# Kernel optimization log

Measured on AMD Instinct MI355X. Metric: run time of the kernel, lower is better.

## Reference

```python
import jax, jax.numpy as jnp
import numpy as np

# ---- static config (mirrors __init__) ----
OMEGAS = [5.0, 7.0, 9.0, 12.0, 16.0, 22.0, 30.0, 40.0]
XI = 0.05
DT = 0.01
UJ_U1 = 0.01

_decay = (1.0 / (2.0 * np.pi * XI)) * np.log(1.0 / UJ_U1)  # cycles to decay to uj_u1
VALID_W = [int(2.0 * np.pi / w / np.sqrt(1.0 - XI ** 2) * _decay / DT) for w in OMEGAS]
KER = [2 * a - 1 for a in VALID_W]  # per-channel duhamel kernel size (odd)
MAXK = max(KER)
OUT_CH = len(OMEGAS)


def _build_irfs(log_omegas):
    """Analytic impulse-response filter bank, shape [OUT_CH, 1, MAXK]."""
    omegas = jnp.clip(jnp.exp(log_omegas), 0.01, 1000.0)
    sq = jnp.sqrt(jnp.float32(1.0 - XI ** 2))
    rows = []
    for i in range(OUT_CH):  # small fixed loop over channels (distinct static lengths)
        W, K = VALID_W[i], KER[i]
        tt = jnp.arange(W, dtype=jnp.float32) * DT
        omegaD = omegas[i] * sq
        irf = (1.0 / omegaD) * jnp.exp(-XI * omegas[i] * tt) * jnp.sin(omegaD * tt)
        w = jnp.concatenate([irf[::-1], jnp.zeros((K // 2,), jnp.float32)])  # len K
        addpad = MAXK - K  # even, since K and MAXK are both odd
        w = jnp.pad(w, (addpad // 2, addpad // 2))
        rows.append(w)
    return jnp.stack(rows)[:, None, :]  # [O, 1, MAXK]


def setup_inputs() -> dict:
    key = jax.random.key(0)
    x = jax.random.normal(key, (16, 1, 65536), dtype=jnp.float32)
    log_omegas = jnp.log(jnp.asarray(OMEGAS, dtype=jnp.float32))
    return {"inputs": x, "log_omegas": log_omegas}


def reference(inputs, log_omegas):
    irfs = _build_irfs(log_omegas)  # [O,1,MAXK]
    pad = MAXK // 2
    xp = jnp.pad(inputs, ((0, 0), (0, 0), (pad, pad)))
    # torch conv1d is cross-correlation == lax conv (no kernel flip)
    return jax.lax.conv_general_dilated(
        xp, irfs, window_strides=(1,), padding='VALID',
        dimension_numbers=('NCH', 'OIH', 'NCH'))
```

## Files before the change

### kernel.cpp

```cpp
#include <hip/hip_runtime.h>
#include <math.h>


#define N_SAMP  65536
#define NB      16
#define NO      8
#define NT      512
#define LBLK    4096
#define LOOKB   3904
#define TQ      2000

constexpr int CW[NO]  = {1844, 1317, 1024, 768, 576, 419, 307, 230};
constexpr int CHS[NO] = {32, 24, 20, 16, 12, 8, 8, 4};

__device__ __forceinline__ int P(int q) { return q ^ ((q >> 3) & 7); }

__device__ __forceinline__ float rfl(float x) {
    return __int_as_float(__builtin_amdgcn_readfirstlane(__float_as_int(x)));
}

template<int O>
__device__ __forceinline__ void duh_wave(const float* __restrict__ lw,
                                         float* __restrict__ out,
                                         const float* __restrict__ tile,
                                         float* __restrict__ yw,
                                         int b, int n0, int lane)
{
    constexpr int W  = CW[O];
    constexpr int Wu = (W + 3) & ~3;
    constexpr int E  = Wu - W;
    constexpr int QW = Wu / 4;
    constexpr int HS = CHS[O];
    constexpr int HQ = HS / 4;

    const float omf  = fminf(fmaxf(__expf(lw[O]), 0.01f), 1000.0f);
    const float omD  = omf * 0.99874921777190895f;
    const float th   = omD * 0.01f;
    const float alph = 0.0005f * omf;
    const float r1   = __expf(-alph);
    const float gr = rfl(r1 * __cosf(th)), gi = rfl(r1 * __sinf(th));
    const float rW   = __expf(-alph * (float)W);
    const float aW   = th * (float)W;
    const float binv = 1.0f / omD;
    const float c1   = rfl(binv);
    const float c2   = rfl(binv * rW * __cosf(aW));
    const float cei  = rfl(-binv * rW * __sinf(aW));

    float g2r_ = gr*gr - gi*gi,         g2i_ = 2.f*gr*gi;
    float g3r_ = g2r_*gr - g2i_*gi,     g3i_ = g2r_*gi + g2i_*gr;
    float g4r_ = g2r_*g2r_ - g2i_*g2i_, g4i_ = 2.f*g2r_*g2i_;
    const float G2r = rfl(g2r_), G2i = rfl(g2i_);
    const float G3r = rfl(g3r_), G3i = rfl(g3i_);
    const float G4r = rfl(g4r_), G4i = rfl(g4i_);

    float Mor[7], Moi[7];
    {
        const float rl = __expf(-alph * 32.f);
        const float al = th * 32.f;
        float pr = rl * __cosf(al), pq = rl * __sinf(al);
#pragma unroll
        for (int k = 0; k < 7; ++k) {
            Mor[k] = rfl(pr); Moi[k] = rfl(pq);
            const float nr = pr*pr - pq*pq, ni = 2.f*pr*pq;
            pr = nr; pq = ni;
        }
    }
    float Mhr[6], Mhi[6];
    {
        const float rl = __expf(-alph * (float)HS);
        const float al = th * (float)HS;
        float pr = rl * __cosf(al), pq = rl * __sinf(al);
#pragma unroll
        for (int k = 0; k < 6; ++k) {
            Mhr[k] = rfl(pr); Mhi[k] = rfl(pq);
            const float nr = pr*pr - pq*pq, ni = 2.f*pr*pq;
            pr = nr; pq = ni;
        }
    }
    float plr = 1.f, pli = 0.f;
#pragma unroll
    for (int k = 0; k < 6; ++k) {
        if ((lane >> k) & 1) {
            const float nr = plr*Mor[k] - pli*Moi[k];
            const float ni = plr*Moi[k] + pli*Mor[k];
            plr = nr; pli = ni;
        }
    }

#define LDQ(q) (*(const float4*)&tile[4 * P(q)])
#define DSEL(e0,e1,e2,e3,d0,dn)                                              \
    if constexpr (E == 0)      { e0=d0.x; e1=d0.y; e2=d0.z; e3=d0.w; }       \
    else if constexpr (E == 1) { e0=d0.y; e1=d0.z; e2=d0.w; e3=dn.x; }       \
    else if constexpr (E == 2) { e0=d0.z; e1=d0.w; e2=dn.x; e3=dn.y; }       \
    else                       { e0=d0.w; e1=dn.x; e2=dn.y; e3=dn.z; }
#define STEP(xa, xc)                                              \
    {                                                             \
        const float er = fmaf(-c2, (xc), c1 * (xa));              \
        const float ei = cei * (xc);                              \
        const float nr = fmaf(gr, Br, fmaf(-gi, Bi, er));         \
        const float ni = fmaf(gi, Br, fmaf( gr, Bi, ei));         \
        Br = nr; Bi = ni;                                         \
    }

    float Cr, Ci;
    {
        float Br = 0.f, Bi = 0.f;
        const int q1 = 976 - 16 * HS + HQ * lane;
        const int q2 = q1 - QW;
        float4 d0 = LDQ(q2);
#pragma unroll
        for (int m = 0; m < HQ; ++m) {
            const float4 s1 = LDQ(q1 + m);
            const float4 dn = LDQ(q2 + m + 1);
            float e0, e1, e2, e3;
            DSEL(e0, e1, e2, e3, d0, dn);
            STEP(s1.x, e0); STEP(s1.y, e1); STEP(s1.z, e2); STEP(s1.w, e3);
            d0 = dn;
        }
        float Sr = Br, Si = Bi;
#pragma unroll
        for (int k = 0; k < 6; ++k) {
            const int d = 1 << k;
            const float ur = __shfl_up(Sr, d, 64);
            const float ui = __shfl_up(Si, d, 64);
            if (lane >= d) {
                const float nr = fmaf(Mhr[k], ur, fmaf(-Mhi[k], ui, Sr));
                const float ni = fmaf(Mhr[k], ui, fmaf( Mhi[k], ur, Si));
                Sr = nr; Si = ni;
            }
        }
        Cr = rfl(__shfl(Sr, 63, 64));
        Ci = rfl(__shfl(Si, 63, 64));
    }

#pragma unroll
    for (int s = 0; s < 2; ++s) {
        const int q1 = 976 + 512 * s + 8 * lane;
        const int q2 = q1 - QW;

        float4 lz[8];
        float Br = 0.f, Bi = 0.f;
        float4 d0 = LDQ(q2);
#pragma unroll
        for (int m = 0; m < 8; ++m) {
            const float4 s1 = LDQ(q1 + m);
            const float4 dn = LDQ(q2 + m + 1);
            float e0, e1, e2, e3;
            DSEL(e0, e1, e2, e3, d0, dn);
            float4 lq;
            STEP(s1.x, e0); lq.x = Bi;
            STEP(s1.y, e1); lq.y = Bi;
            STEP(s1.z, e2); lq.z = Bi;
            STEP(s1.w, e3); lq.w = Bi;
            lz[m] = lq;
            d0 = dn;
        }

        float Sr = Br, Si = Bi;
#pragma unroll
        for (int k = 0; k < 6; ++k) {
            const int d = 1 << k;
            const float ur = __shfl_up(Sr, d, 64);
            const float ui = __shfl_up(Si, d, 64);
            if (lane >= d) {
                const float nr = fmaf(Mor[k], ur, fmaf(-Moi[k], ui, Sr));
                const float ni = fmaf(Mor[k], ui, fmaf( Moi[k], ur, Si));
                Sr = nr; Si = ni;
            }
        }
        const float Tr = __shfl(Sr, 63, 64);
        const float Ti = __shfl(Si, 63, 64);
        float exr = __shfl_up(Sr, 1, 64);
        float exi = __shfl_up(Si, 1, 64);
        if (lane == 0) { exr = 0.f; exi = 0.f; }

        const float sr = fmaf(plr, Cr, fmaf(-pli, Ci, exr));
        const float si = fmaf(plr, Ci, fmaf( pli, Cr, exi));

        float wr = fmaf(gr, sr, -(gi * si));
        float wi = fmaf(gi, sr,  (gr * si));
#pragma unroll
        for (int m = 0; m < 8; ++m) {
            float4 y;
            y.x = lz[m].x + wi;
            y.y = fmaf(gi,  wr, fmaf(gr,  wi, lz[m].y));
            y.z = fmaf(G2i, wr, fmaf(G2r, wi, lz[m].z));
            y.w = fmaf(G3i, wr, fmaf(G3r, wi, lz[m].w));
            *(float4*)&yw[4 * P(8 * lane + m)] = y;
            const float nwr = fmaf(G4r, wr, -(G4i * wi));
            const float nwi = fmaf(G4i, wr,  (G4r * wi));
            wr = nwr; wi = nwi;
        }
        float* op = out + ((size_t)(b * NO + O)) * (size_t)N_SAMP
                        + n0 + s * 2048;
#pragma unroll
        for (int i = 0; i < 8; ++i) {
            const int q = 64 * i + lane;
            const float4 v = *(const float4*)&yw[4 * P(q)];
            *(float4*)(op + 4 * q) = v;
        }

        const float nCr = fmaf(Mor[6], Cr, fmaf(-Moi[6], Ci, Tr));
        const float nCi = fmaf(Mor[6], Ci, fmaf( Moi[6], Cr, Ti));
        Cr = rfl(nCr); Ci = rfl(nCi);
    }
#undef STEP
#undef DSEL
#undef LDQ
}

__global__ __launch_bounds__(NT, 2)
void duh_kernel(const float* __restrict__ x, const float* __restrict__ lw,
                float* __restrict__ out)
{
    __shared__ float tile[TQ * 4];
    __shared__ float ybuf[NO * 2048];
    const int c  = blockIdx.x;
    const int b  = blockIdx.y;
    const int n0 = c * LBLK;
    const int t  = threadIdx.x;

    const float* xb = x + (size_t)b * N_SAMP;
    const int tstart = n0 - LOOKB;
#pragma unroll
    for (int i = 0; i < 4; ++i) {
        const int k = t + 512 * i;
        if (k < TQ) {
            const int g0 = tstart + 4 * k;
            float4 v;
            if (g0 >= 0) v = *(const float4*)(xb + g0);
            else { v.x = 0.f; v.y = 0.f; v.z = 0.f; v.w = 0.f; }
            *(float4*)&tile[4 * P(k)] = v;
        }
    }
    __syncthreads();

    const int wv   = t >> 6;
    const int lane = t & 63;
    float* yw = ybuf + wv * 2048;
    switch (wv) {
      case 0: duh_wave<0>(lw, out, tile, yw, b, n0, lane); break;
      case 1: duh_wave<1>(lw, out, tile, yw, b, n0, lane); break;
      case 2: duh_wave<2>(lw, out, tile, yw, b, n0, lane); break;
      case 3: duh_wave<3>(lw, out, tile, yw, b, n0, lane); break;
      case 4: duh_wave<4>(lw, out, tile, yw, b, n0, lane); break;
      case 5: duh_wave<5>(lw, out, tile, yw, b, n0, lane); break;
      case 6: duh_wave<6>(lw, out, tile, yw, b, n0, lane); break;
      default:duh_wave<7>(lw, out, tile, yw, b, n0, lane); break;
    }
}

extern "C" void kernel_launch(void* const* d_in, const int* in_sizes, int n_in,
                              void* d_out, int out_size, void* d_ws, size_t ws_size,
                              hipStream_t stream) {
    const float* x  = (const float*)d_in[0];
    const float* lw = (const float*)d_in[1];
    float* out = (float*)d_out;

    dim3 grid(N_SAMP / LBLK, NB);
    duh_kernel<<<grid, dim3(NT), 0, stream>>>(x, lw, out);
}
```

Measured before the change: 16.69 us.

## Split tile load into two phases overlapping global loads with coefficient setup

Moves the input tile load into each wave's function, issuing all global loads up front and then overlapping their latency with the per-channel coefficient and power computation. The lookback half of the tile is written and barriered before the carry scan, and the main half is written only after that scan, so its load latency is hidden further. This adds a second block barrier and more bounds checks on the loads, and the barriers inside the per-wave switch rely on every wave reaching them.

```diff
diff --git a/kernel.cpp b/kernel.cpp
--- a/kernel.cpp
+++ b/kernel.cpp
@@ -21,10 +21,11 @@
 
 template<int O>
 __device__ __forceinline__ void duh_wave(const float* __restrict__ lw,
+                                         const float* __restrict__ xb,
                                          float* __restrict__ out,
-                                         const float* __restrict__ tile,
+                                         float* __restrict__ tile,
                                          float* __restrict__ yw,
-                                         int b, int n0, int lane)
+                                         int b, int n0, int t, int lane)
 {
     constexpr int W  = CW[O];
     constexpr int Wu = (W + 3) & ~3;
@@ -32,6 +33,28 @@
     constexpr int QW = Wu / 4;
     constexpr int HS = CHS[O];
     constexpr int HQ = HS / 4;
+
+    const int tstart = n0 - LOOKB;
+
+    auto ldg = [&](int k) -> float4 {
+        const int g0 = tstart + 4 * k;
+        float4 v;
+        if (g0 >= 0 && g0 + 3 < N_SAMP) {
+            v = *(const float4*)(xb + g0);
+        } else {
+            v.x = (g0 + 0 >= 0 && g0 + 0 < N_SAMP) ? xb[g0 + 0] : 0.0f;
+            v.y = (g0 + 1 >= 0 && g0 + 1 < N_SAMP) ? xb[g0 + 1] : 0.0f;
+            v.z = (g0 + 2 >= 0 && g0 + 2 < N_SAMP) ? xb[g0 + 2] : 0.0f;
+            v.w = (g0 + 3 >= 0 && g0 + 3 < N_SAMP) ? xb[g0 + 3] : 0.0f;
+        }
+        return v;
+    };
+    const bool hasA1 = (t < 464);
+    const float4 vA0 = ldg(t);
+    float4 vA1;
+    if (hasA1) vA1 = ldg(512 + t);
+    const float4 vB0 = ldg(976 + t);
+    const float4 vB1 = ldg(1488 + t);
 
     const float omf  = fminf(fmaxf(__expf(lw[O]), 0.01f), 1000.0f);
     const float omD  = omf * 0.99874921777190895f;
@@ -86,6 +109,11 @@
             plr = nr; pli = ni;
         }
     }
+
+    *(float4*)&tile[4 * P(t)] = vA0;
+    if (hasA1) *(float4*)&tile[4 * P(512 + t)] = vA1;
+    asm volatile("s_waitcnt lgkmcnt(0)" ::: "memory");
+    __builtin_amdgcn_s_barrier();
 
 #define LDQ(q) (*(const float4*)&tile[4 * P(q)])
 #define DSEL(e0,e1,e2,e3,d0,dn)                                              \
@@ -133,6 +161,11 @@
         Ci = rfl(__shfl(Si, 63, 64));
     }
 
+    *(float4*)&tile[4 * P(976 + t)]  = vB0;
+    *(float4*)&tile[4 * P(1488 + t)] = vB1;
+    asm volatile("s_waitcnt lgkmcnt(0)" ::: "memory");
+    __builtin_amdgcn_s_barrier();
+
 #pragma unroll
     for (int s = 0; s < 2; ++s) {
         const int q1 = 976 + 512 * s + 8 * lane;
@@ -219,34 +252,19 @@
     const int b  = blockIdx.y;
     const int n0 = c * LBLK;
     const int t  = threadIdx.x;
-
-    const float* xb = x + (size_t)b * N_SAMP;
-    const int tstart = n0 - LOOKB;
-#pragma unroll
-    for (int i = 0; i < 4; ++i) {
-        const int k = t + 512 * i;
-        if (k < TQ) {
-            const int g0 = tstart + 4 * k;
-            float4 v;
-            if (g0 >= 0) v = *(const float4*)(xb + g0);
-            else { v.x = 0.f; v.y = 0.f; v.z = 0.f; v.w = 0.f; }
-            *(float4*)&tile[4 * P(k)] = v;
-        }
-    }
-    __syncthreads();
-
     const int wv   = t >> 6;
     const int lane = t & 63;
+    const float* xb = x + (size_t)b * N_SAMP;
     float* yw = ybuf + wv * 2048;
     switch (wv) {
-      case 0: duh_wave<0>(lw, out, tile, yw, b, n0, lane); break;
-      case 1: duh_wave<1>(lw, out, tile, yw, b, n0, lane); break;
-      case 2: duh_wave<2>(lw, out, tile, yw, b, n0, lane); break;
-      case 3: duh_wave<3>(lw, out, tile, yw, b, n0, lane); break;
-      case 4: duh_wave<4>(lw, out, tile, yw, b, n0, lane); break;
-      case 5: duh_wave<5>(lw, out, tile, yw, b, n0, lane); break;
-      case 6: duh_wave<6>(lw, out, tile, yw, b, n0, lane); break;
-      default:duh_wave<7>(lw, out, tile, yw, b, n0, lane); break;
+      case 0: duh_wave<0>(lw, xb, out, tile, yw, b, n0, t, lane); break;
+      case 1: duh_wave<1>(lw, xb, out, tile, yw, b, n0, t, lane); break;
+      case 2: duh_wave<2>(lw, xb, out, tile, yw, b, n0, t, lane); break;
+      case 3: duh_wave<3>(lw, xb, out, tile, yw, b, n0, t, lane); break;
+      case 4: duh_wave<4>(lw, xb, out, tile, yw, b, n0, t, lane); break;
+      case 5: duh_wave<5>(lw, xb, out, tile, yw, b, n0, t, lane); break;
+      case 6: duh_wave<6>(lw, xb, out, tile, yw, b, n0, t, lane); break;
+      default:duh_wave<7>(lw, xb, out, tile, yw, b, n0, t, lane); break;
     }
 }
 
```

New measurement: 17.49 us. 1.05x slower.
